# Performance work log

Hardware: AMD Instinct MI355X
Metric: run time of the kernel (lower is better)

Reference implementation:

```python
import jax, jax.numpy as jnp
import numpy as np

N, E, DIN, D, NUM_LAYERS = 50000, 800000, 64, 128, 3


def setup_inputs() -> dict:
    key = jax.random.key(0)
    ks = jax.random.split(key, 16)
    s = lambda fan_in: 1.0 / np.sqrt(fan_in)
    inp = {
        "x": jax.random.normal(ks[0], (N, DIN), jnp.float32),
        "edge_index": jax.random.randint(ks[1], (2, E), 0, N, jnp.int64),
        "edge_attr": jax.random.normal(ks[2], (E,), jnp.float32),
        "batch": jnp.zeros((N,), jnp.int64),
        # embed: Linear(DIN, D)
        "W_embed": jax.random.uniform(ks[3], (DIN, D), jnp.float32, -s(DIN), s(DIN)),
        "b_embed": jax.random.uniform(ks[4], (D,), jnp.float32, -s(DIN), s(DIN)),
        # msg_snd: Linear(D, D)
        "W_snd": jax.random.uniform(ks[5], (D, D), jnp.float32, -s(D), s(D)),
        "b_snd": jax.random.uniform(ks[6], (D,), jnp.float32, -s(D), s(D)),
        # msg_rec: Linear(2D, 2D)
        "W_rec": jax.random.uniform(ks[7], (2 * D, 2 * D), jnp.float32, -s(2 * D), s(2 * D)),
        "b_rec": jax.random.uniform(ks[8], (2 * D,), jnp.float32, -s(2 * D), s(2 * D)),
        # GRUCell(input=2D, hidden=D): gates ordered (r, z, n) as in torch
        "W_ih": jax.random.uniform(ks[9], (2 * D, 3 * D), jnp.float32, -s(D), s(D)),
        "b_ih": jax.random.uniform(ks[10], (3 * D,), jnp.float32, -s(D), s(D)),
        "W_hh": jax.random.uniform(ks[11], (D, 3 * D), jnp.float32, -s(D), s(D)),
        "b_hh": jax.random.uniform(ks[12], (3 * D,), jnp.float32, -s(D), s(D)),
    }
    return inp


def reference(x, edge_index, edge_attr, batch, W_embed, b_embed, W_snd, b_snd,
              W_rec, b_rec, W_ih, b_ih, W_hh, b_hh):
    n_nodes = x.shape[0]
    row, col = edge_index[0], edge_index[1]
    ea = edge_attr[:, None]                                    # [E,1]
    # scatter_mean denominator: in-degree, clamped to 1
    cnt = jax.ops.segment_sum(jnp.ones_like(edge_attr), col, num_segments=n_nodes)
    cnt = jnp.maximum(cnt, 1.0)[:, None]                       # [N,1]

    h = x @ W_embed + b_embed                                  # [N,D]
    for _ in range(NUM_LAYERS):
        s = jax.nn.leaky_relu(h @ W_snd + b_snd)               # msg_snd, [N,D]
        msgs = s[row] * ea                                     # gather + weight, [E,D]
        agg = jax.ops.segment_sum(msgs, col, num_segments=n_nodes) / cnt  # scatter_mean
        m = jax.nn.leaky_relu(jnp.concatenate([agg, h], -1) @ W_rec + b_rec)  # [N,2D]
        # torch GRUCell
        gi = m @ W_ih + b_ih                                   # [N,3D]
        gh = h @ W_hh + b_hh                                   # [N,3D]
        ir, iz, inn = jnp.split(gi, 3, axis=-1)
        hr, hz, hn = jnp.split(gh, 3, axis=-1)
        r = jax.nn.sigmoid(ir + hr)
        z = jax.nn.sigmoid(iz + hz)
        n = jnp.tanh(inn + r * hn)
        h = (1.0 - z) * n + z * h
    return h
```

## Files before the change

### kernel.cpp

```cpp
#include <hip/hip_runtime.h>
#include <hip/hip_bf16.h>
#include <stdint.h>

using bf16 = __hip_bfloat16;
typedef __attribute__((ext_vector_type(8))) short short8;
typedef __attribute__((ext_vector_type(4))) float f32x4;

#define LRELU_SLOPE 0.01f

#define GLOAD_LDS16(g, l) __builtin_amdgcn_global_load_lds( \
    (const __attribute__((address_space(1))) void*)(g),     \
    (__attribute__((address_space(3))) void*)(l), 16, 0, 0)

__global__ __launch_bounds__(256) void gemm_tile_kernel(
    const bf16* __restrict__ A, int lda,
    const bf16* __restrict__ BT,
    const float* __restrict__ bias,
    bf16* __restrict__ C, int ldc,
    float* __restrict__ Cf, int ldcf,
    int N, int K, int act)
{
    __shared__ bf16 smem[8192];
    bf16* As = smem;
    bf16* Bs = smem + 4096;

    const int t    = threadIdx.x;
    const int wv   = t >> 6;
    const int ln   = t & 63;
    const int m16  = ln & 15;
    const int q    = ln >> 4;
    const int row0 = blockIdx.x * 128;
    const int col0 = blockIdx.y * 128;
    const int wr   = (wv & 1) * 64;
    const int wc   = (wv >> 1) * 64;

    const int srow   = t >> 2;
    const int schunk = (t & 3) * 8;

    int ra0 = row0 + srow;       if (ra0 > N - 1) ra0 = N - 1;
    int ra1 = row0 + 64 + srow;  if (ra1 > N - 1) ra1 = N - 1;
    const bf16* gA0 = A  + (size_t)ra0 * lda + schunk;
    const bf16* gA1 = A  + (size_t)ra1 * lda + schunk;
    const bf16* gB0 = BT + (size_t)(col0 + srow)      * K + schunk;
    const bf16* gB1 = BT + (size_t)(col0 + 64 + srow) * K + schunk;

    f32x4 acc[4][4];
#pragma unroll
    for (int mi = 0; mi < 4; ++mi)
#pragma unroll
        for (int ni = 0; ni < 4; ++ni)
            acc[mi][ni] = (f32x4){0.f, 0.f, 0.f, 0.f};

    for (int k0 = 0; k0 < K; k0 += 32) {
        GLOAD_LDS16(gA0 + k0, As +        wv * 512);
        GLOAD_LDS16(gA1 + k0, As + 2048 + wv * 512);
        GLOAD_LDS16(gB0 + k0, Bs +        wv * 512);
        GLOAD_LDS16(gB1 + k0, Bs + 2048 + wv * 512);
        __syncthreads();

        short8 a[4], b[4];
#pragma unroll
        for (int mi = 0; mi < 4; ++mi)
            a[mi] = *reinterpret_cast<const short8*>(As + (wr + mi * 16 + m16) * 32 + q * 8);
#pragma unroll
        for (int ni = 0; ni < 4; ++ni)
            b[ni] = *reinterpret_cast<const short8*>(Bs + (wc + ni * 16 + m16) * 32 + q * 8);
#pragma unroll
        for (int mi = 0; mi < 4; ++mi)
#pragma unroll
            for (int ni = 0; ni < 4; ++ni)
                acc[mi][ni] = __builtin_amdgcn_mfma_f32_16x16x32_bf16(
                    a[mi], b[ni], acc[mi][ni], 0, 0, 0);
        __syncthreads();
    }

#pragma unroll
    for (int mi = 0; mi < 4; ++mi) {
        int rbase = row0 + wr + mi * 16 + q * 4;
#pragma unroll
        for (int ni = 0; ni < 4; ++ni) {
            int col = col0 + wc + ni * 16 + m16;
            float bv = bias[col];
#pragma unroll
            for (int r = 0; r < 4; ++r) {
                int row = rbase + r;
                if (row < N) {
                    float v = acc[mi][ni][r] + bv;
                    if (act) v = (v > 0.f) ? v : LRELU_SLOPE * v;
                    C[(size_t)row * ldc + col] = __float2bfloat16(v);
                    if (Cf) Cf[(size_t)row * ldcf + col] = v;
                }
            }
        }
    }
}

__global__ void prep_kernel(const float* __restrict__ x, bf16* __restrict__ xb, int nx,
                            const float* __restrict__ W0, bf16* __restrict__ T0,
                            const float* __restrict__ W1, bf16* __restrict__ T1,
                            const float* __restrict__ W2, bf16* __restrict__ T2,
                            const float* __restrict__ W3, bf16* __restrict__ T3,
                            const float* __restrict__ W4, bf16* __restrict__ T4)
{
    int t = blockIdx.x * 256 + threadIdx.x;
    if (t < nx) { xb[t] = __float2bfloat16(x[t]); return; }
    t -= nx;
    if (t < 8192)  { T0[(size_t)(t % 128) * 64  + t / 128] = __float2bfloat16(W0[t]); return; }
    t -= 8192;
    if (t < 16384) { T1[(size_t)(t % 128) * 128 + t / 128] = __float2bfloat16(W1[t]); return; }
    t -= 16384;
    if (t < 65536) { T2[(size_t)(t % 256) * 256 + t / 256] = __float2bfloat16(W2[t]); return; }
    t -= 65536;
    if (t < 98304) { T3[(size_t)(t % 384) * 256 + t / 384] = __float2bfloat16(W3[t]); return; }
    t -= 98304;
    if (t < 49152) { T4[(size_t)(t % 384) * 128 + t / 384] = __float2bfloat16(W4[t]); return; }
}

__global__ void hist_kernel(const int* __restrict__ col, int* __restrict__ cnt, int E)
{
    int e = blockIdx.x * 256 + threadIdx.x;
    if (e < E) atomicAdd(&cnt[col[e]], 1);
}

__global__ void blockscan_kernel(const int* __restrict__ cnt, int* __restrict__ off,
                                 int* __restrict__ bsum, int N)
{
    __shared__ int sm[256];
    int i = blockIdx.x * 256 + threadIdx.x;
    int v = (i < N) ? cnt[i] : 0;
    sm[threadIdx.x] = v;
    __syncthreads();
    for (int d = 1; d < 256; d <<= 1) {
        int tv = (threadIdx.x >= (unsigned)d) ? sm[threadIdx.x - d] : 0;
        __syncthreads();
        sm[threadIdx.x] += tv;
        __syncthreads();
    }
    if (i < N) off[i] = sm[threadIdx.x] - v;
    if (threadIdx.x == 255) bsum[blockIdx.x] = sm[255];
}

__global__ void bscan_kernel(int* __restrict__ bsum, int nb)
{
    __shared__ int sm[512];
    int v = (threadIdx.x < (unsigned)nb) ? bsum[threadIdx.x] : 0;
    sm[threadIdx.x] = v;
    __syncthreads();
    for (int d = 1; d < 512; d <<= 1) {
        int tv = (threadIdx.x >= (unsigned)d) ? sm[threadIdx.x - d] : 0;
        __syncthreads();
        sm[threadIdx.x] += tv;
        __syncthreads();
    }
    if (threadIdx.x < (unsigned)nb) bsum[threadIdx.x] = sm[threadIdx.x] - v;
}

__global__ void addoff_kernel(int* __restrict__ off, const int* __restrict__ bsum,
                              const int* __restrict__ cnt, float* __restrict__ icnt,
                              int N, int E)
{
    int i = blockIdx.x * 256 + threadIdx.x;
    if (i < N) {
        off[i] += bsum[blockIdx.x];
        icnt[i] = 1.0f / fmaxf((float)cnt[i], 1.0f);
    }
    if (i == 0) off[N] = E;
}

__global__ void fill_kernel(const int* __restrict__ row, const int* __restrict__ col,
                            const float* __restrict__ ea, const int* __restrict__ off,
                            int* __restrict__ fil, int* __restrict__ row_s,
                            float* __restrict__ ea_s, int E)
{
    int e = blockIdx.x * 256 + threadIdx.x;
    if (e < E) {
        int c = col[e];
        int p = atomicAdd(&fil[c], 1);
        int pos = off[c] + p;
        row_s[pos] = row[e];
        ea_s[pos]  = ea[e];
    }
}

__global__ void agg_kernel(const int* __restrict__ off,
                           const int* __restrict__ row_s,
                           const float* __restrict__ ea_s,
                           const bf16* __restrict__ s,
                           const float* __restrict__ icnt,
                           bf16* __restrict__ cat, int N)
{
    int wid  = (int)((blockIdx.x * blockDim.x + threadIdx.x) >> 6);
    int lane = threadIdx.x & 63;
    if (wid >= N) return;
    const int rg = lane >> 4;
    const int cl = lane & 15;
    int b = off[wid], e = off[wid + 1];

    float acc[8];
#pragma unroll
    for (int j = 0; j < 8; ++j) acc[j] = 0.f;

    for (int i = b + rg; i < e; i += 4) {
        int   r = row_s[i];
        float w = ea_s[i];
        short8 v = *reinterpret_cast<const short8*>(s + (size_t)r * 128 + cl * 8);
#pragma unroll
        for (int j = 0; j < 8; ++j) {
            union { uint32_t u; float f; } cv;
            cv.u = ((uint32_t)(uint16_t)v[j]) << 16;
            acc[j] += w * cv.f;
        }
    }
#pragma unroll
    for (int j = 0; j < 8; ++j) {
        acc[j] += __shfl_xor(acc[j], 16, 64);
        acc[j] += __shfl_xor(acc[j], 32, 64);
    }
    if (rg == 0) {
        float ic = icnt[wid];
        short8 o;
#pragma unroll
        for (int j = 0; j < 8; ++j) {
            bf16 hv = __float2bfloat16(acc[j] * ic);
            o[j] = *reinterpret_cast<short*>(&hv);
        }
        *reinterpret_cast<short8*>(cat + (size_t)wid * 256 + cl * 8) = o;
    }
}

__global__ void gru_kernel(const bf16* __restrict__ gi,
                           const bf16* __restrict__ gh,
                           float* __restrict__ h,
                           bf16* __restrict__ hb,
                           int N)
{
    int t = blockIdx.x * 256 + threadIdx.x;
    if (t >= N * 16) return;
    int v = t >> 4, c = (t & 15) * 8;
    const bf16* gp = gi + (size_t)v * 384 + c;
    const bf16* hp = gh + (size_t)v * 384 + c;
    short8 ir8 = *reinterpret_cast<const short8*>(gp);
    short8 iz8 = *reinterpret_cast<const short8*>(gp + 128);
    short8 in8 = *reinterpret_cast<const short8*>(gp + 256);
    short8 hr8 = *reinterpret_cast<const short8*>(hp);
    short8 hz8 = *reinterpret_cast<const short8*>(hp + 128);
    short8 hn8 = *reinterpret_cast<const short8*>(hp + 256);
    float* hv = h + (size_t)v * 128 + c;
    f32x4 h0 = *reinterpret_cast<f32x4*>(hv);
    f32x4 h1 = *reinterpret_cast<f32x4*>(hv + 4);

    auto b2f = [](short s) {
        union { uint32_t u; float f; } cv;
        cv.u = ((uint32_t)(uint16_t)s) << 16;
        return cv.f;
    };

    f32x4 o0, o1;
    short8 ob;
#pragma unroll
    for (int j = 0; j < 8; ++j) {
        float r  = 1.f / (1.f + __expf(-(b2f(ir8[j]) + b2f(hr8[j]))));
        float z  = 1.f / (1.f + __expf(-(b2f(iz8[j]) + b2f(hz8[j]))));
        float n  = tanhf(b2f(in8[j]) + r * b2f(hn8[j]));
        float hvj = (j < 4) ? h0[j] : h1[j - 4];
        float hn_ = (1.f - z) * n + z * hvj;
        if (j < 4) o0[j] = hn_; else o1[j - 4] = hn_;
        bf16 hbv = __float2bfloat16(hn_);
        ob[j] = *reinterpret_cast<short*>(&hbv);
    }
    *reinterpret_cast<f32x4*>(hv)     = o0;
    *reinterpret_cast<f32x4*>(hv + 4) = o1;
    *reinterpret_cast<short8*>(hb + (size_t)v * 256 + c) = ob;
}

extern "C" void kernel_launch(void* const* d_in, const int* in_sizes, int n_in,
                              void* d_out, int out_size, void* d_ws, size_t ws_size,
                              hipStream_t stream)
{
    const float* x       = (const float*)d_in[0];
    const int*   ei      = (const int*)d_in[1];
    const float* ea      = (const float*)d_in[2];
    const float* W_embed = (const float*)d_in[4];
    const float* b_embed = (const float*)d_in[5];
    const float* W_snd   = (const float*)d_in[6];
    const float* b_snd   = (const float*)d_in[7];
    const float* W_rec   = (const float*)d_in[8];
    const float* b_rec   = (const float*)d_in[9];
    const float* W_ih    = (const float*)d_in[10];
    const float* b_ih    = (const float*)d_in[11];
    const float* W_hh    = (const float*)d_in[12];
    const float* b_hh    = (const float*)d_in[13];

    const int N = in_sizes[3];
    const int E = in_sizes[2];

    float* hout = (float*)d_out;

    char* p = (char*)d_ws;
    auto carve = [&](size_t bytes) {
        char* r = p;
        p += (bytes + 255) & ~(size_t)255;
        return (void*)r;
    };
    bf16*  xb    = (bf16*) carve((size_t)N * 64 * 2);
    bf16*  cat   = (bf16*) carve((size_t)N * 256 * 2);
    bf16*  sbuf  = (bf16*) carve((size_t)N * 128 * 2);
    bf16*  mbuf  = (bf16*) carve((size_t)N * 256 * 2);
    bf16*  ghbuf = sbuf;
    bf16*  gibuf = (bf16*) carve((size_t)N * 384 * 2);
    int*   cnt   = (int*)  carve((size_t)N * 4);
    int*   fil   = (int*)  carve((size_t)N * 4);
    int*   off   = (int*)  carve((size_t)(N + 1) * 4);
    int*   bsum  = (int*)  carve((size_t)512 * 4);
    float* icnt  = (float*)carve((size_t)N * 4);
    int*   row_s = (int*)  carve((size_t)E * 4);
    float* ea_s  = (float*)carve((size_t)E * 4);
    bf16*  wtE   = (bf16*) carve((size_t)128 * 64 * 2);
    bf16*  wtS   = (bf16*) carve((size_t)128 * 128 * 2);
    bf16*  wtR   = (bf16*) carve((size_t)256 * 256 * 2);
    bf16*  wtI   = (bf16*) carve((size_t)384 * 256 * 2);
    bf16*  wtH   = (bf16*) carve((size_t)384 * 128 * 2);

    const int* rowp = ei;
    const int* colp = ei + E;

    hipMemsetAsync(cnt, 0, (size_t)N * 4, stream);
    hipMemsetAsync(fil, 0, (size_t)N * 4, stream);

    const int TB = 256;
    auto nb = [](int n) { return (n + 255) / 256; };

    prep_kernel<<<nb(N * 64 + 237568), TB, 0, stream>>>(
        x, xb, N * 64,
        W_embed, wtE, W_snd, wtS, W_rec, wtR, W_ih, wtI, W_hh, wtH);

    hist_kernel<<<nb(E), TB, 0, stream>>>(colp, cnt, E);
    blockscan_kernel<<<nb(N), TB, 0, stream>>>(cnt, off, bsum, N);
    bscan_kernel<<<1, 512, 0, stream>>>(bsum, nb(N));
    addoff_kernel<<<nb(N), TB, 0, stream>>>(off, bsum, cnt, icnt, N, E);
    fill_kernel<<<nb(E), TB, 0, stream>>>(rowp, colp, ea, off, fil, row_s, ea_s, E);

    auto gemm = [&](const bf16* Ap, int lda, const bf16* BTp, const float* bp,
                    bf16* Cp, int ldc, float* Cfp, int ldcf,
                    int K, int Dout, int act) {
        dim3 g((N + 127) / 128, Dout / 128);
        gemm_tile_kernel<<<g, TB, 0, stream>>>(Ap, lda, BTp, bp, Cp, ldc,
                                               Cfp, ldcf, N, K, act);
    };

    gemm(xb, 64, wtE, b_embed, cat + 128, 256, hout, 128, 64, 128, 0);

    for (int L = 0; L < 3; ++L) {
        gemm(cat + 128, 256, wtS, b_snd, sbuf, 128, nullptr, 0, 128, 128, 1);
        agg_kernel<<<(N * 64 + TB - 1) / TB, TB, 0, stream>>>(off, row_s, ea_s,
                                                              sbuf, icnt, cat, N);
        gemm(cat, 256, wtR, b_rec, mbuf, 256, nullptr, 0, 256, 256, 1);
        gemm(mbuf, 256, wtI, b_ih, gibuf, 384, nullptr, 0, 256, 384, 0);
        gemm(cat + 128, 256, wtH, b_hh, ghbuf, 384, nullptr, 0, 128, 384, 0);
        gru_kernel<<<nb(N * 16), TB, 0, stream>>>(gibuf, ghbuf, hout, cat + 128, N);
    }
}
```

Baseline: 699.0 us.

## Fuse GRU input/hidden GEMMs with gate math and restructure GEMM tiling

Replaces the two separate GRU GEMMs and the elementwise GRU kernel with one fused kernel. It concatenates [m, h] into a 384-wide buffer and multiplies by a combined, zero-padded weight with pre-summed biases, then applies the gates from LDS. The generic GEMM becomes a 64-row tile that loads the whole A panel into swizzled LDS once and reads B directly from global memory without per-k barriers. Edge row indices and weights are packed into int2 so aggregation needs one load per edge. The point is to cut intermediate gi/gh round trips and launches, at the cost of the padded weight adding some redundant MFMA work and heavier LDS use.

```diff
diff --git a/kernel.cpp b/kernel.cpp
--- a/kernel.cpp
+++ b/kernel.cpp
@@ -12,74 +12,78 @@
     (const __attribute__((address_space(1))) void*)(g),     \
     (__attribute__((address_space(3))) void*)(l), 16, 0, 0)
 
-__global__ __launch_bounds__(256) void gemm_tile_kernel(
+__device__ __forceinline__ float b2f(short s) {
+    union { uint32_t u; float f; } cv;
+    cv.u = ((uint32_t)(uint16_t)s) << 16;
+    return cv.f;
+}
+__device__ __forceinline__ short f2b(float f) {
+    bf16 h = __float2bfloat16(f);
+    return *reinterpret_cast<short*>(&h);
+}
+
+__global__ __launch_bounds__(256) void gemm_m64_kernel(
     const bf16* __restrict__ A, int lda,
     const bf16* __restrict__ BT,
     const float* __restrict__ bias,
     bf16* __restrict__ C, int ldc,
     float* __restrict__ Cf, int ldcf,
-    int N, int K, int act)
-{
-    __shared__ bf16 smem[8192];
-    bf16* As = smem;
-    bf16* Bs = smem + 4096;
-
-    const int t    = threadIdx.x;
-    const int wv   = t >> 6;
-    const int ln   = t & 63;
-    const int m16  = ln & 15;
-    const int q    = ln >> 4;
-    const int row0 = blockIdx.x * 128;
-    const int col0 = blockIdx.y * 128;
-    const int wr   = (wv & 1) * 64;
-    const int wc   = (wv >> 1) * 64;
-
-    const int srow   = t >> 2;
-    const int schunk = (t & 3) * 8;
-
-    int ra0 = row0 + srow;       if (ra0 > N - 1) ra0 = N - 1;
-    int ra1 = row0 + 64 + srow;  if (ra1 > N - 1) ra1 = N - 1;
-    const bf16* gA0 = A  + (size_t)ra0 * lda + schunk;
-    const bf16* gA1 = A  + (size_t)ra1 * lda + schunk;
-    const bf16* gB0 = BT + (size_t)(col0 + srow)      * K + schunk;
-    const bf16* gB1 = BT + (size_t)(col0 + 64 + srow) * K + schunk;
-
-    f32x4 acc[4][4];
-#pragma unroll
-    for (int mi = 0; mi < 4; ++mi)
+    bf16* __restrict__ C2, int ldc2,
+    int N, int K, int cprShift, int act)
+{
+    __shared__ bf16 As[64 * 256];
+    const int t   = threadIdx.x;
+    const int wv  = t >> 6, ln = t & 63, m16 = ln & 15, q = ln >> 4;
+    const int row0 = blockIdx.x * 64;
+    const int col0 = blockIdx.y * 128 + (wv >> 1) * 64;
+    const int wr   = (wv & 1) * 32;
+    const int cmask = (1 << cprShift) - 1;
+    const int trips = (1 << cprShift) >> 2;
+
+    for (int i = 0; i < trips; ++i) {
+        int g    = i * 256 + t;
+        int row  = g >> cprShift;
+        int cidx = (g & cmask) ^ (row & cmask);
+        int grow = row0 + row; if (grow > N - 1) grow = N - 1;
+        GLOAD_LDS16(A + (size_t)grow * lda + cidx * 8,
+                    As + ((i * 256 + wv * 64) << 3));
+    }
+    __syncthreads();
+
+    f32x4 acc[2][4];
+#pragma unroll
+    for (int mi = 0; mi < 2; ++mi)
 #pragma unroll
         for (int ni = 0; ni < 4; ++ni)
             acc[mi][ni] = (f32x4){0.f, 0.f, 0.f, 0.f};
 
     for (int k0 = 0; k0 < K; k0 += 32) {
-        GLOAD_LDS16(gA0 + k0, As +        wv * 512);
-        GLOAD_LDS16(gA1 + k0, As + 2048 + wv * 512);
-        GLOAD_LDS16(gB0 + k0, Bs +        wv * 512);
-        GLOAD_LDS16(gB1 + k0, Bs + 2048 + wv * 512);
-        __syncthreads();
-
-        short8 a[4], b[4];
-#pragma unroll
-        for (int mi = 0; mi < 4; ++mi)
-            a[mi] = *reinterpret_cast<const short8*>(As + (wr + mi * 16 + m16) * 32 + q * 8);
+        int cbase = (k0 >> 3) + q;
+        short8 a[2], b[4];
+#pragma unroll
+        for (int mi = 0; mi < 2; ++mi) {
+            int row = wr + mi * 16 + m16;
+            int cs  = cbase ^ (row & cmask);
+            a[mi] = *reinterpret_cast<const short8*>(As + row * K + cs * 8);
+        }
 #pragma unroll
         for (int ni = 0; ni < 4; ++ni)
-            b[ni] = *reinterpret_cast<const short8*>(Bs + (wc + ni * 16 + m16) * 32 + q * 8);
-#pragma unroll
-        for (int mi = 0; mi < 4; ++mi)
+            b[ni] = *reinterpret_cast<const short8*>(
+                BT + (size_t)(col0 + ni * 16 + m16) * K + k0 + q * 8);
+#pragma unroll
+        for (int mi = 0; mi < 2; ++mi)
 #pragma unroll
             for (int ni = 0; ni < 4; ++ni)
                 acc[mi][ni] = __builtin_amdgcn_mfma_f32_16x16x32_bf16(
                     a[mi], b[ni], acc[mi][ni], 0, 0, 0);
-        __syncthreads();
-    }
-
-#pragma unroll
-    for (int mi = 0; mi < 4; ++mi) {
+    }
+
+#pragma unroll
+    for (int mi = 0; mi < 2; ++mi) {
         int rbase = row0 + wr + mi * 16 + q * 4;
 #pragma unroll
         for (int ni = 0; ni < 4; ++ni) {
-            int col = col0 + wc + ni * 16 + m16;
+            int col = col0 + ni * 16 + m16;
             float bv = bias[col];
 #pragma unroll
             for (int r = 0; r < 4; ++r) {
@@ -89,31 +93,160 @@
                     if (act) v = (v > 0.f) ? v : LRELU_SLOPE * v;
                     C[(size_t)row * ldc + col] = __float2bfloat16(v);
                     if (Cf) Cf[(size_t)row * ldcf + col] = v;
+                    if (C2) C2[(size_t)row * ldc2 + col] = __float2bfloat16(v);
                 }
             }
         }
     }
 }
 
+__global__ __launch_bounds__(256) void fused_gru_kernel(
+    const bf16* __restrict__ MH,
+    const bf16* __restrict__ WT,
+    const float* __restrict__ bext,
+    float* __restrict__ h32,
+    bf16* __restrict__ catH,
+    bf16* __restrict__ mhH,
+    int N)
+{
+    __shared__ bf16 smem[32768];
+    const int t  = threadIdx.x;
+    const int wv = t >> 6, ln = t & 63, m16 = ln & 15, q = ln >> 4;
+    const int row0 = blockIdx.x * 64;
+
+    for (int i = 0; i < 12; ++i) {
+        int g    = i * 256 + t;
+        int row  = g / 48;
+        int cpos = g - row * 48;
+        int cidx = cpos ^ (row & 15);
+        GLOAD_LDS16(MH + (size_t)(row0 + row) * 384 + cidx * 8,
+                    smem + ((i * 256 + wv * 64) << 3));
+    }
+    __syncthreads();
+
+    const int kbeg = (wv == 3) ? 256 : 0;
+    const int kend = (wv == 2) ? 256 : 384;
+    const int colw = wv << 7;
+
+    f32x4 acc[4][8];
+#pragma unroll
+    for (int mi = 0; mi < 4; ++mi)
+#pragma unroll
+        for (int ni = 0; ni < 8; ++ni)
+            acc[mi][ni] = (f32x4){0.f, 0.f, 0.f, 0.f};
+
+    for (int k0 = kbeg; k0 < kend; k0 += 32) {
+        int cbase = (k0 >> 3) + q;
+        short8 a[4], b[8];
+#pragma unroll
+        for (int mi = 0; mi < 4; ++mi) {
+            int row = mi * 16 + m16;
+            int cs  = cbase ^ m16;
+            a[mi] = *reinterpret_cast<const short8*>(smem + row * 384 + cs * 8);
+        }
+#pragma unroll
+        for (int ni = 0; ni < 8; ++ni)
+            b[ni] = *reinterpret_cast<const short8*>(
+                WT + (size_t)(colw + ni * 16 + m16) * 384 + k0 + q * 8);
+#pragma unroll
+        for (int mi = 0; mi < 4; ++mi)
+#pragma unroll
+            for (int ni = 0; ni < 8; ++ni)
+                acc[mi][ni] = __builtin_amdgcn_mfma_f32_16x16x32_bf16(
+                    a[mi], b[ni], acc[mi][ni], 0, 0, 0);
+    }
+    __syncthreads();
+
+    {
+        bf16* X = smem + (wv << 13);
+#pragma unroll
+        for (int mi = 0; mi < 4; ++mi) {
+#pragma unroll
+            for (int ni = 0; ni < 8; ++ni) {
+                int ch = ni * 16 + m16;
+                float bv = bext[colw + ch];
+                int sw = (((mi << 2) + q) ^ m16) << 2;
+                union { uint2 u2; short s4[4]; } pk;
+#pragma unroll
+                for (int r = 0; r < 4; ++r) pk.s4[r] = f2b(acc[mi][ni][r] + bv);
+                *reinterpret_cast<uint2*>(X + ch * 64 + sw) = pk.u2;
+            }
+        }
+    }
+    __syncthreads();
+
+    const bf16* Xr  = smem;
+    const bf16* Xz  = smem + 8192;
+    const bf16* Xin = smem + 16384;
+    const bf16* Xhn = smem + 24576;
+
+#pragma unroll
+    for (int rc = 0; rc < 4; ++rc) {
+        int rc4  = (wv << 2) + rc;
+        int rloc = rc4 << 2;
+#pragma unroll
+        for (int c2 = 0; c2 < 2; ++c2) {
+            int ch = (c2 << 6) + ln;
+            int sw = (rc4 ^ (ch & 15)) << 2;
+            union { uint2 u2; short s4[4]; } pr, pz, pi, ph;
+            pr.u2 = *reinterpret_cast<const uint2*>(Xr  + ch * 64 + sw);
+            pz.u2 = *reinterpret_cast<const uint2*>(Xz  + ch * 64 + sw);
+            pi.u2 = *reinterpret_cast<const uint2*>(Xin + ch * 64 + sw);
+            ph.u2 = *reinterpret_cast<const uint2*>(Xhn + ch * 64 + sw);
+#pragma unroll
+            for (int r = 0; r < 4; ++r) {
+                int row = row0 + rloc + r;
+                if (row < N) {
+                    float hv = h32[(size_t)row * 128 + ch];
+                    float rr = 1.f / (1.f + __expf(-b2f(pr.s4[r])));
+                    float zz = 1.f / (1.f + __expf(-b2f(pz.s4[r])));
+                    float nn = tanhf(b2f(pi.s4[r]) + rr * b2f(ph.s4[r]));
+                    float hnew = (1.f - zz) * nn + zz * hv;
+                    h32[(size_t)row * 128 + ch] = hnew;
+                    short hb = f2b(hnew);
+                    catH[(size_t)row * 256 + ch] = *reinterpret_cast<bf16*>(&hb);
+                    mhH[(size_t)row * 384 + ch]  = *reinterpret_cast<bf16*>(&hb);
+                }
+            }
+        }
+    }
+}
+
 __global__ void prep_kernel(const float* __restrict__ x, bf16* __restrict__ xb, int nx,
-                            const float* __restrict__ W0, bf16* __restrict__ T0,
-                            const float* __restrict__ W1, bf16* __restrict__ T1,
-                            const float* __restrict__ W2, bf16* __restrict__ T2,
-                            const float* __restrict__ W3, bf16* __restrict__ T3,
-                            const float* __restrict__ W4, bf16* __restrict__ T4)
+                            const float* __restrict__ W_embed, bf16* __restrict__ TE,
+                            const float* __restrict__ W_snd,   bf16* __restrict__ TS,
+                            const float* __restrict__ W_rec,   bf16* __restrict__ TM,
+                            const float* __restrict__ W_ih, const float* __restrict__ W_hh,
+                            bf16* __restrict__ TX,
+                            const float* __restrict__ b_ih, const float* __restrict__ b_hh,
+                            float* __restrict__ bext)
 {
     int t = blockIdx.x * 256 + threadIdx.x;
     if (t < nx) { xb[t] = __float2bfloat16(x[t]); return; }
     t -= nx;
-    if (t < 8192)  { T0[(size_t)(t % 128) * 64  + t / 128] = __float2bfloat16(W0[t]); return; }
+    if (t < 8192)  { TE[(t % 128) * 64  + t / 128] = __float2bfloat16(W_embed[t]); return; }
     t -= 8192;
-    if (t < 16384) { T1[(size_t)(t % 128) * 128 + t / 128] = __float2bfloat16(W1[t]); return; }
+    if (t < 16384) { TS[(t % 128) * 128 + t / 128] = __float2bfloat16(W_snd[t]); return; }
     t -= 16384;
-    if (t < 65536) { T2[(size_t)(t % 256) * 256 + t / 256] = __float2bfloat16(W2[t]); return; }
+    if (t < 65536) { TM[(t % 256) * 256 + t / 256] = __float2bfloat16(W_rec[t]); return; }
     t -= 65536;
-    if (t < 98304) { T3[(size_t)(t % 384) * 256 + t / 384] = __float2bfloat16(W3[t]); return; }
-    t -= 98304;
-    if (t < 49152) { T4[(size_t)(t % 384) * 128 + t / 384] = __float2bfloat16(W4[t]); return; }
+    if (t < 196608) {
+        int c = t / 384, k = t - c * 384;
+        float v;
+        if (c < 256)      v = (k < 256) ? W_ih[k * 384 + c] : W_hh[(k - 256) * 384 + c];
+        else if (c < 384) v = (k < 256) ? W_ih[k * 384 + c] : 0.f;
+        else              v = (k < 256) ? 0.f : W_hh[(k - 256) * 384 + (c - 128)];
+        TX[t] = __float2bfloat16(v);
+        return;
+    }
+    t -= 196608;
+    if (t < 512) {
+        float v;
+        if (t < 256)      v = b_ih[t] + b_hh[t];
+        else if (t < 384) v = b_ih[t];
+        else              v = b_hh[t - 128];
+        bext[t] = v;
+    }
 }
 
 __global__ void hist_kernel(const int* __restrict__ col, int* __restrict__ cnt, int E)
@@ -169,22 +302,19 @@
 
 __global__ void fill_kernel(const int* __restrict__ row, const int* __restrict__ col,
                             const float* __restrict__ ea, const int* __restrict__ off,
-                            int* __restrict__ fil, int* __restrict__ row_s,
-                            float* __restrict__ ea_s, int E)
+                            int* __restrict__ fil, int2* __restrict__ re, int E)
 {
     int e = blockIdx.x * 256 + threadIdx.x;
     if (e < E) {
         int c = col[e];
         int p = atomicAdd(&fil[c], 1);
-        int pos = off[c] + p;
-        row_s[pos] = row[e];
-        ea_s[pos]  = ea[e];
+        int2 v; v.x = row[e]; v.y = __float_as_int(ea[e]);
+        re[off[c] + p] = v;
     }
 }
 
 __global__ void agg_kernel(const int* __restrict__ off,
-                           const int* __restrict__ row_s,
-                           const float* __restrict__ ea_s,
+                           const int2* __restrict__ re,
                            const bf16* __restrict__ s,
                            const float* __restrict__ icnt,
                            bf16* __restrict__ cat, int N)
@@ -201,15 +331,11 @@
     for (int j = 0; j < 8; ++j) acc[j] = 0.f;
 
     for (int i = b + rg; i < e; i += 4) {
-        int   r = row_s[i];
-        float w = ea_s[i];
-        short8 v = *reinterpret_cast<const short8*>(s + (size_t)r * 128 + cl * 8);
-#pragma unroll
-        for (int j = 0; j < 8; ++j) {
-            union { uint32_t u; float f; } cv;
-            cv.u = ((uint32_t)(uint16_t)v[j]) << 16;
-            acc[j] += w * cv.f;
-        }
+        int2 pr = re[i];
+        float w = __int_as_float(pr.y);
+        short8 v = *reinterpret_cast<const short8*>(s + (size_t)pr.x * 128 + cl * 8);
+#pragma unroll
+        for (int j = 0; j < 8; ++j) acc[j] += w * b2f(v[j]);
     }
 #pragma unroll
     for (int j = 0; j < 8; ++j) {
@@ -220,57 +346,9 @@
         float ic = icnt[wid];
         short8 o;
 #pragma unroll
-        for (int j = 0; j < 8; ++j) {
-            bf16 hv = __float2bfloat16(acc[j] * ic);
-            o[j] = *reinterpret_cast<short*>(&hv);
-        }
+        for (int j = 0; j < 8; ++j) o[j] = f2b(acc[j] * ic);
         *reinterpret_cast<short8*>(cat + (size_t)wid * 256 + cl * 8) = o;
     }
-}
-
-__global__ void gru_kernel(const bf16* __restrict__ gi,
-                           const bf16* __restrict__ gh,
-                           float* __restrict__ h,
-                           bf16* __restrict__ hb,
-                           int N)
-{
-    int t = blockIdx.x * 256 + threadIdx.x;
-    if (t >= N * 16) return;
-    int v = t >> 4, c = (t & 15) * 8;
-    const bf16* gp = gi + (size_t)v * 384 + c;
-    const bf16* hp = gh + (size_t)v * 384 + c;
-    short8 ir8 = *reinterpret_cast<const short8*>(gp);
-    short8 iz8 = *reinterpret_cast<const short8*>(gp + 128);
-    short8 in8 = *reinterpret_cast<const short8*>(gp + 256);
-    short8 hr8 = *reinterpret_cast<const short8*>(hp);
-    short8 hz8 = *reinterpret_cast<const short8*>(hp + 128);
-    short8 hn8 = *reinterpret_cast<const short8*>(hp + 256);
-    float* hv = h + (size_t)v * 128 + c;
-    f32x4 h0 = *reinterpret_cast<f32x4*>(hv);
-    f32x4 h1 = *reinterpret_cast<f32x4*>(hv + 4);
-
-    auto b2f = [](short s) {
-        union { uint32_t u; float f; } cv;
-        cv.u = ((uint32_t)(uint16_t)s) << 16;
-        return cv.f;
-    };
-
-    f32x4 o0, o1;
-    short8 ob;
-#pragma unroll
-    for (int j = 0; j < 8; ++j) {
-        float r  = 1.f / (1.f + __expf(-(b2f(ir8[j]) + b2f(hr8[j]))));
-        float z  = 1.f / (1.f + __expf(-(b2f(iz8[j]) + b2f(hz8[j]))));
-        float n  = tanhf(b2f(in8[j]) + r * b2f(hn8[j]));
-        float hvj = (j < 4) ? h0[j] : h1[j - 4];
-        float hn_ = (1.f - z) * n + z * hvj;
-        if (j < 4) o0[j] = hn_; else o1[j - 4] = hn_;
-        bf16 hbv = __float2bfloat16(hn_);
-        ob[j] = *reinterpret_cast<short*>(&hbv);
-    }
-    *reinterpret_cast<f32x4*>(hv)     = o0;
-    *reinterpret_cast<f32x4*>(hv + 4) = o1;
-    *reinterpret_cast<short8*>(hb + (size_t)v * 256 + c) = ob;
 }
 
 extern "C" void kernel_launch(void* const* d_in, const int* in_sizes, int n_in,
@@ -293,6 +371,7 @@
 
     const int N = in_sizes[3];
     const int E = in_sizes[2];
+    const int N64 = ((N + 63) / 64) * 64;
 
     float* hout = (float*)d_out;
 
@@ -302,24 +381,21 @@
         p += (bytes + 255) & ~(size_t)255;
         return (void*)r;
     };
-    bf16*  xb    = (bf16*) carve((size_t)N * 64 * 2);
-    bf16*  cat   = (bf16*) carve((size_t)N * 256 * 2);
-    bf16*  sbuf  = (bf16*) carve((size_t)N * 128 * 2);
-    bf16*  mbuf  = (bf16*) carve((size_t)N * 256 * 2);
-    bf16*  ghbuf = sbuf;
-    bf16*  gibuf = (bf16*) carve((size_t)N * 384 * 2);
-    int*   cnt   = (int*)  carve((size_t)N * 4);
-    int*   fil   = (int*)  carve((size_t)N * 4);
-    int*   off   = (int*)  carve((size_t)(N + 1) * 4);
-    int*   bsum  = (int*)  carve((size_t)512 * 4);
-    float* icnt  = (float*)carve((size_t)N * 4);
-    int*   row_s = (int*)  carve((size_t)E * 4);
-    float* ea_s  = (float*)carve((size_t)E * 4);
-    bf16*  wtE   = (bf16*) carve((size_t)128 * 64 * 2);
-    bf16*  wtS   = (bf16*) carve((size_t)128 * 128 * 2);
-    bf16*  wtR   = (bf16*) carve((size_t)256 * 256 * 2);
-    bf16*  wtI   = (bf16*) carve((size_t)384 * 256 * 2);
-    bf16*  wtH   = (bf16*) carve((size_t)384 * 128 * 2);
+    bf16*  xb   = (bf16*) carve((size_t)N64 * 64  * 2);
+    bf16*  cat  = (bf16*) carve((size_t)N64 * 256 * 2);
+    bf16*  mh   = (bf16*) carve((size_t)N64 * 384 * 2);
+    bf16*  sbuf = (bf16*) carve((size_t)N64 * 128 * 2);
+    int2*  re   = (int2*) carve((size_t)E * 8);
+    int*   cnt  = (int*)  carve((size_t)N * 4);
+    int*   fil  = (int*)  carve((size_t)N * 4);
+    int*   off  = (int*)  carve((size_t)(N + 1) * 4);
+    int*   bsum = (int*)  carve((size_t)512 * 4);
+    float* icnt = (float*)carve((size_t)N * 4);
+    bf16*  wtE  = (bf16*) carve((size_t)128 * 64 * 2);
+    bf16*  wtS  = (bf16*) carve((size_t)128 * 128 * 2);
+    bf16*  wtM  = (bf16*) carve((size_t)256 * 256 * 2);
+    bf16*  wtX  = (bf16*) carve((size_t)512 * 384 * 2);
+    float* bext = (float*)carve((size_t)512 * 4);
 
     const int* rowp = ei;
     const int* colp = ei + E;
@@ -330,33 +406,37 @@
     const int TB = 256;
     auto nb = [](int n) { return (n + 255) / 256; };
 
-    prep_kernel<<<nb(N * 64 + 237568), TB, 0, stream>>>(
-        x, xb, N * 64,
-        W_embed, wtE, W_snd, wtS, W_rec, wtR, W_ih, wtI, W_hh, wtH);
+    prep_kernel<<<nb(N * 64 + 287232), TB, 0, stream>>>(
+        x, xb, N * 64, W_embed, wtE, W_snd, wtS, W_rec, wtM,
+        W_ih, W_hh, wtX, b_ih, b_hh, bext);
 
     hist_kernel<<<nb(E), TB, 0, stream>>>(colp, cnt, E);
     blockscan_kernel<<<nb(N), TB, 0, stream>>>(cnt, off, bsum, N);
     bscan_kernel<<<1, 512, 0, stream>>>(bsum, nb(N));
     addoff_kernel<<<nb(N), TB, 0, stream>>>(off, bsum, cnt, icnt, N, E);
-    fill_kernel<<<nb(E), TB, 0, stream>>>(rowp, colp, ea, off, fil, row_s, ea_s, E);
-
+    fill_kernel<<<nb(E), TB, 0, stream>>>(rowp, colp, ea, off, fil, re, E);
+
+    const int gx = (N + 63) / 64;
     auto gemm = [&](const bf16* Ap, int lda, const bf16* BTp, const float* bp,
                     bf16* Cp, int ldc, float* Cfp, int ldcf,
-                    int K, int Dout, int act) {
-        dim3 g((N + 127) / 128, Dout / 128);
-        gemm_tile_kernel<<<g, TB, 0, stream>>>(Ap, lda, BTp, bp, Cp, ldc,
-                                               Cfp, ldcf, N, K, act);
+                    bf16* C2p, int ldc2, int K, int shift, int Dout, int act) {
+        dim3 g(gx, Dout / 128);
+        gemm_m64_kernel<<<g, TB, 0, stream>>>(Ap, lda, BTp, bp, Cp, ldc,
+                                              Cfp, ldcf, C2p, ldc2,
+                                              N, K, shift, act);
     };
 
-    gemm(xb, 64, wtE, b_embed, cat + 128, 256, hout, 128, 64, 128, 0);
+    gemm(xb, 64, wtE, b_embed, cat + 128, 256, hout, 128, mh + 256, 384,
+         64, 3, 128, 0);
 
     for (int L = 0; L < 3; ++L) {
-        gemm(cat + 128, 256, wtS, b_snd, sbuf, 128, nullptr, 0, 128, 128, 1);
-        agg_kernel<<<(N * 64 + TB - 1) / TB, TB, 0, stream>>>(off, row_s, ea_s,
-                                                              sbuf, icnt, cat, N);
-        gemm(cat, 256, wtR, b_rec, mbuf, 256, nullptr, 0, 256, 256, 1);
-        gemm(mbuf, 256, wtI, b_ih, gibuf, 384, nullptr, 0, 256, 384, 0);
-        gemm(cat + 128, 256, wtH, b_hh, ghbuf, 384, nullptr, 0, 128, 384, 0);
-        gru_kernel<<<nb(N * 16), TB, 0, stream>>>(gibuf, ghbuf, hout, cat + 128, N);
-    }
-}
+        gemm(cat + 128, 256, wtS, b_snd, sbuf, 128, nullptr, 0, nullptr, 0,
+             128, 4, 128, 1);
+        agg_kernel<<<(N * 64 + TB - 1) / TB, TB, 0, stream>>>(off, re, sbuf,
+                                                              icnt, cat, N);
+        gemm(cat, 256, wtM, b_rec, mh, 384, nullptr, 0, nullptr, 0,
+             256, 5, 256, 1);
+        fused_gru_kernel<<<gx, TB, 0, stream>>>(mh, wtX, bext, hout,
+                                                cat + 128, mh + 256, N);
+    }
+}
```

Result: slower. 788.7 us (+12.8%).
